# Kernel optimization log

Measured on AMD Instinct MI355X. Metric: run time of the kernel, lower is better.

Reference implementation:

```python
import jax, jax.numpy as jnp
import numpy as np

D = 128          # node feature dim (input_dim)
ATT_NUM = 2      # number of attention heads (att_num)
ATT_TIMES = 2    # attention refinement iterations (att_times)
K = 1            # interact_dim from att_style 'ntn_1'
DIN2 = D * ATT_NUM   # NTN input dim = 256
FMAP = 16        # feature_map_dim
B = 8            # number of graph pairs
N = 100000       # nodes per graph
EPS = 1e-12      # F.normalize eps


def _glorot(key, shape):
    fan_in, fan_out = shape[-1], shape[-2] if len(shape) > 1 else shape[-1]
    std = np.sqrt(2.0 / (fan_in + fan_out)).astype(np.float32)
    return jax.random.normal(key, shape, dtype=jnp.float32) * std


def setup_inputs() -> dict:
    key = jax.random.key(0)
    ks = jax.random.split(key, 16)
    inp = {
        "x1": jax.random.normal(ks[0], (B, N, D), dtype=jnp.float32),
        "x2": jax.random.normal(ks[1], (B, N, D), dtype=jnp.float32),
        # Attention params (stacked over att_num heads)
        "W_att": _glorot(ks[2], (ATT_NUM, D, D)),
        "V_att": _glorot(ks[3], (ATT_NUM, K, 2 * D)),
        "Wt_att": _glorot(ks[4], (ATT_NUM, K, D, D)),
        "U_att": _glorot(ks[5], (ATT_NUM, K, 1)),
        "b_att": jax.random.normal(ks[6], (ATT_NUM, K), dtype=jnp.float32) * 0.1,
        # NTN params
        "V_ntn": _glorot(ks[7], (FMAP, 2 * DIN2)),
        "W_ntn": _glorot(ks[8], (FMAP, DIN2, DIN2)),
        "b_ntn": jax.random.normal(ks[9], (FMAP,), dtype=jnp.float32),
        # projection MLP: 16 -> 8 -> 4 -> 2 -> 1 (Linear, no bias; weight shape (out, in))
        "proj0": _glorot(ks[10], (8, 16)),
        "proj1": _glorot(ks[11], (4, 8)),
        "proj2": _glorot(ks[12], (2, 4)),
        "proj3": _glorot(ks[13], (1, 2)),
    }
    return inp


def _l1_normalize(s, axis):
    return s / jnp.maximum(jnp.sum(jnp.abs(s), axis=axis, keepdims=True), EPS)


def _attention(x, W_att, V_att, Wt_att, U_att, b_att):
    # x: (N, D)  ->  pooled graph embedding (D * ATT_NUM,)
    outs = []
    for i in range(ATT_NUM):
        xc = x
        out = None
        Va, Vb = V_att[i, :, :D], V_att[i, :, D:]   # (K, D) each
        for _ in range(ATT_TIMES):
            h = jnp.tanh(jnp.mean(xc, axis=0) @ W_att[i])        # (D,)
            # NTN-style attention scores, vectorized over all nodes
            s = xc @ Va.T + (Vb @ h)[None, :]                    # (N, K)
            s = s + jnp.einsum('nd,kde,e->nk', xc, Wt_att[i], h)
            s = s + b_att[i][None, :]
            s = _l1_normalize(s, axis=1)
            att = jax.nn.sigmoid(s) @ U_att[i]                   # (N, 1)
            out = att[:, 0] @ xc                                 # (D,)
            xc = xc * att
        outs.append(out)
    return jnp.concatenate(outs)   # (DIN2,)


def _ntn(g1, g2, V_ntn, W_ntn, b_ntn):
    # g1, g2: (DIN2,) -> (FMAP,)
    Va, Vb = V_ntn[:, :DIN2], V_ntn[:, DIN2:]
    s = Va @ g1 + Vb @ g2 + jnp.einsum('fde,d,e->f', W_ntn, g1, g2) + b_ntn
    s = s / jnp.maximum(jnp.sum(jnp.abs(s)), EPS)   # L1 normalize over the single row
    return jax.nn.relu(s)


def reference(x1, x2, W_att, V_att, Wt_att, U_att, b_att,
              V_ntn, W_ntn, b_ntn, proj0, proj1, proj2, proj3):
    def pair_fn(xa, xb):
        g1 = _attention(xa, W_att, V_att, Wt_att, U_att, b_att)
        g2 = _attention(xb, W_att, V_att, Wt_att, U_att, b_att)
        y = _ntn(g1, g2, V_ntn, W_ntn, b_ntn)      # (FMAP,)
        for Wp in (proj0, proj1, proj2, proj3):
            y = Wp @ y
        return y                                    # (1,)
    return jax.vmap(pair_fn)(x1, x2)                # (B, 1) pairwise similarity scores
```

## Files before the change

kernel.cpp:

```cpp
#include <hip/hip_runtime.h>
#include <hip/hip_bf16.h>
#include <math.h>

#define NROWS 100000
#define DIM 128
#define NGRAPH 16
#define NCHUNK 128
#define CHROWS 782
#define EPSV 1e-12f

#define SZ_SUMP (NGRAPH*NCHUNK*DIM)
#define SZ_WV   (NGRAPH*2*DIM)
#define SZ_OP   (NGRAPH*NCHUNK*2*DIM)
#define OFF_SUMP 0
#define OFF_WV1 (OFF_SUMP + SZ_SUMP)
#define OFF_C1  (OFF_WV1 + SZ_WV)
#define OFF_O1P (OFF_C1 + 32)
#define OFF_WV2 (OFF_O1P + SZ_OP)
#define OFF_C2  (OFF_WV2 + SZ_WV)
#define OFF_O2P (OFF_C2 + 32)
#define OFF_S   (OFF_O2P + SZ_OP)

typedef float v4f __attribute__((ext_vector_type(4)));

__device__ __forceinline__ const float* graph_ptr(const float* x1, const float* x2, int g) {
    return (g < 8) ? (x1 + (size_t)g * NROWS * DIM) : (x2 + (size_t)(g - 8) * NROWS * DIM);
}

__device__ __forceinline__ float4 ldnt4(const float* p) {
    v4f v = __builtin_nontemporal_load(reinterpret_cast<const v4f*>(p));
    return make_float4(v.x, v.y, v.z, v.w);
}

__device__ __forceinline__ float4 ld4(const float* p) {
    return *reinterpret_cast<const float4*>(p);
}

__device__ __forceinline__ float red16(float x) {
    int t;
    t = __builtin_amdgcn_update_dpp(0, __float_as_int(x), 0xB1, 0xF, 0xF, true);
    x += __int_as_float(t);
    t = __builtin_amdgcn_update_dpp(0, __float_as_int(x), 0x4E, 0xF, 0xF, true);
    x += __int_as_float(t);
    t = __builtin_amdgcn_update_dpp(0, __float_as_int(x), 0x141, 0xF, 0xF, true);
    x += __int_as_float(t);
    t = __builtin_amdgcn_update_dpp(0, __float_as_int(x), 0x140, 0xF, 0xF, true);
    x += __int_as_float(t);
    return x;
}

__device__ __forceinline__ float dot8(float4 v0, float4 v1, float4 w0, float4 w1) {
    float d = v0.x * w0.x;
    d = fmaf(v0.y, w0.y, d); d = fmaf(v0.z, w0.z, d); d = fmaf(v0.w, w0.w, d);
    d = fmaf(v1.x, w1.x, d); d = fmaf(v1.y, w1.y, d); d = fmaf(v1.z, w1.z, d);
    d = fmaf(v1.w, w1.w, d);
    return d;
}

__device__ __forceinline__ void acc4(float4& a, float f, float4 v) {
    a.x = fmaf(f, v.x, a.x); a.y = fmaf(f, v.y, a.y);
    a.z = fmaf(f, v.z, a.z); a.w = fmaf(f, v.w, a.w);
}

__global__ __launch_bounds__(256, 8) void k_sum(const float* __restrict__ x1,
                                                const float* __restrict__ x2,
                                                float* __restrict__ sump) {
    int g = blockIdx.x >> 7, c = blockIdx.x & (NCHUNK - 1);
    const float* xg = graph_ptr(x1, x2, g);
    int lane = threadIdx.x & 31, grp = threadIdx.x >> 5;
    int col = lane * 4;
    float ax = 0.f, ay = 0.f, az = 0.f, aw = 0.f;
    int r0 = c * CHROWS, r1 = min(r0 + CHROWS, NROWS);
    int r = r0 + grp;
    for (; r + 24 < r1; r += 32) {
        float4 a = ldnt4(xg + (size_t)r * DIM + col);
        float4 b = ldnt4(xg + (size_t)(r + 8) * DIM + col);
        float4 d = ldnt4(xg + (size_t)(r + 16) * DIM + col);
        float4 e = ldnt4(xg + (size_t)(r + 24) * DIM + col);
        ax += a.x; ay += a.y; az += a.z; aw += a.w;
        ax += b.x; ay += b.y; az += b.z; aw += b.w;
        ax += d.x; ay += d.y; az += d.z; aw += d.w;
        ax += e.x; ay += e.y; az += e.z; aw += e.w;
    }
    for (; r < r1; r += 8) {
        float4 a = ldnt4(xg + (size_t)r * DIM + col);
        ax += a.x; ay += a.y; az += a.z; aw += a.w;
    }
    __shared__ float4 lds[256];
    lds[threadIdx.x] = make_float4(ax, ay, az, aw);
    __syncthreads();
    if (threadIdx.x < 32) {
        float4 t = lds[threadIdx.x];
        for (int k = 1; k < 8; ++k) {
            float4 o = lds[k * 32 + threadIdx.x];
            t.x += o.x; t.y += o.y; t.z += o.z; t.w += o.w;
        }
        *reinterpret_cast<float4*>(sump + ((size_t)g * NCHUNK + c) * DIM + threadIdx.x * 4) = t;
    }
}

__global__ __launch_bounds__(256) void k_prep(const float* __restrict__ src, int phase,
                                              const float* __restrict__ W_att,
                                              const float* __restrict__ V_att,
                                              const float* __restrict__ Wt_att,
                                              const float* __restrict__ b_att,
                                              float* __restrict__ wv, float* __restrict__ cc) {
    int g = blockIdx.x >> 1, i = blockIdx.x & 1;
    int tid = threadIdx.x, t = tid & 127, half = tid >> 7;
    __shared__ float mean[DIM], h[DIM], red2[256];
    __shared__ float wt[DIM][DIM + 1];
    const float* Wt = Wt_att + (size_t)i * DIM * DIM;
    for (int idx = tid; idx < DIM * DIM; idx += 256)
        wt[idx >> 7][idx & 127] = Wt[idx];
    float s = 0.f;
    if (phase == 1) {
        for (int c = half; c < NCHUNK; c += 2) s += src[((size_t)g * NCHUNK + c) * DIM + t];
    } else {
        for (int c = half; c < NCHUNK; c += 2) s += src[(((size_t)g * NCHUNK + c) * 2 + i) * DIM + t];
    }
    red2[tid] = s; __syncthreads();
    if (half == 0) mean[t] = (red2[t] + red2[t + 128]) * (1.f / (float)NROWS);
    __syncthreads();
    const float* W = W_att + (size_t)i * DIM * DIM;
    float hv = 0.f;
    for (int d = half * 64; d < half * 64 + 64; ++d) hv = fmaf(mean[d], W[d * DIM + t], hv);
    red2[tid] = hv; __syncthreads();
    if (half == 0) h[t] = tanhf(red2[t] + red2[t + 128]);
    __syncthreads();
    float w = 0.f;
    for (int e = half * 64; e < half * 64 + 64; ++e) w = fmaf(wt[t][e], h[e], w);
    red2[tid] = w; __syncthreads();
    const float* Va = V_att + (size_t)i * 2 * DIM;
    if (half == 0) wv[((size_t)g * 2 + i) * DIM + t] = Va[t] + red2[t] + red2[t + 128];
    __syncthreads();
    if (half == 0) red2[t] = Va[DIM + t] * h[t];
    __syncthreads();
    for (int k = 64; k; k >>= 1) {
        if (tid < k) red2[tid] += red2[tid + k];
        __syncthreads();
    }
    if (tid == 0) cc[g * 2 + i] = red2[0] + b_att[i];
}

__device__ __forceinline__ void body2(float4 v0, float4 v1,
                                      float4 w0a, float4 w0b, float4 w1a, float4 w1b,
                                      float cc0, float cc1,
                                      float ap0, float an0, float ap1, float an1,
                                      float4& a0l, float4& a0h, float4& a1l, float4& a1h) {
    float d0 = red16(dot8(v0, v1, w0a, w0b));
    float d1 = red16(dot8(v0, v1, w1a, w1b));
    float at0 = (d0 + cc0 >= 0.f) ? ap0 : an0;
    float at1 = (d1 + cc1 >= 0.f) ? ap1 : an1;
    acc4(a0l, at0, v0); acc4(a0h, at0, v1);
    acc4(a1l, at1, v0); acc4(a1h, at1, v1);
}

__global__ __launch_bounds__(256, 6) void k_pass2(const float* __restrict__ x1,
                                                  const float* __restrict__ x2,
                                                  const float* __restrict__ wv1,
                                                  const float* __restrict__ c1,
                                                  const float* __restrict__ U_att,
                                                  float* __restrict__ o1p) {
    int g = blockIdx.x >> 7, c = blockIdx.x & (NCHUNK - 1);
    const float* xg = graph_ptr(x1, x2, g);
    int tid = threadIdx.x;
    int l16 = tid & 15, slot = tid >> 4;
    int cb = l16 * 4;
    float4 w0a = ld4(wv1 + ((size_t)g * 2 + 0) * DIM + cb);
    float4 w0b = ld4(wv1 + ((size_t)g * 2 + 0) * DIM + 64 + cb);
    float4 w1a = ld4(wv1 + ((size_t)g * 2 + 1) * DIM + cb);
    float4 w1b = ld4(wv1 + ((size_t)g * 2 + 1) * DIM + 64 + cb);
    float cc0 = c1[g * 2 + 0], cc1 = c1[g * 2 + 1];
    float u0 = U_att[0], u1 = U_att[1];
    float sp = 1.f / (1.f + expf(-1.f)), sn = 1.f / (1.f + expf(1.f));
    float ap0 = u0 * sp, an0 = u0 * sn, ap1 = u1 * sp, an1 = u1 * sn;
    float4 a0l = make_float4(0, 0, 0, 0), a0h = make_float4(0, 0, 0, 0);
    float4 a1l = make_float4(0, 0, 0, 0), a1h = make_float4(0, 0, 0, 0);
    int r0 = c * CHROWS, r1 = min(r0 + CHROWS, NROWS);
    int r = r0 + slot;
    for (; r + 16 < r1; r += 32) {
        const float* p = xg + (size_t)r * DIM + cb;
        const float* q = xg + (size_t)(r + 16) * DIM + cb;
        float4 v0 = ldnt4(p), v1 = ldnt4(p + 64);
        float4 y0 = ldnt4(q), y1 = ldnt4(q + 64);
        body2(v0, v1, w0a, w0b, w1a, w1b, cc0, cc1, ap0, an0, ap1, an1, a0l, a0h, a1l, a1h);
        body2(y0, y1, w0a, w0b, w1a, w1b, cc0, cc1, ap0, an0, ap1, an1, a0l, a0h, a1l, a1h);
    }
    for (; r < r1; r += 16) {
        const float* p = xg + (size_t)r * DIM + cb;
        float4 v0 = ldnt4(p), v1 = ldnt4(p + 64);
        body2(v0, v1, w0a, w0b, w1a, w1b, cc0, cc1, ap0, an0, ap1, an1, a0l, a0h, a1l, a1h);
    }
    __shared__ float red[2][16][DIM];
    *reinterpret_cast<float4*>(&red[0][slot][cb]) = a0l;
    *reinterpret_cast<float4*>(&red[0][slot][64 + cb]) = a0h;
    *reinterpret_cast<float4*>(&red[1][slot][cb]) = a1l;
    *reinterpret_cast<float4*>(&red[1][slot][64 + cb]) = a1h;
    __syncthreads();
    int i = tid >> 7, d = tid & 127;
    float s = 0.f;
    #pragma unroll
    for (int k = 0; k < 16; ++k) s += red[i][k][d];
    o1p[(((size_t)g * NCHUNK + c) * 2 + i) * DIM + d] = s;
}

__device__ __forceinline__ void body3(float4 v0, float4 v1,
                                      float4 wA0a, float4 wA0b, float4 wA1a, float4 wA1b,
                                      float4 wB0a, float4 wB0b, float4 wB1a, float4 wB1b,
                                      float cA0, float cA1, float cB0, float cB1,
                                      float ap0, float an0, float ap1, float an1,
                                      float4& a0l, float4& a0h, float4& a1l, float4& a1h) {
    float dA0 = red16(dot8(v0, v1, wA0a, wA0b));
    float dA1 = red16(dot8(v0, v1, wA1a, wA1b));
    float dB0 = red16(dot8(v0, v1, wB0a, wB0b));
    float dB1 = red16(dot8(v0, v1, wB1a, wB1b));
    float at10 = (dA0 + cA0 >= 0.f) ? ap0 : an0;
    float at11 = (dA1 + cA1 >= 0.f) ? ap1 : an1;
    float at20 = (fmaf(at10, dB0, cB0) >= 0.f) ? ap0 : an0;
    float at21 = (fmaf(at11, dB1, cB1) >= 0.f) ? ap1 : an1;
    float f0 = at10 * at20, f1 = at11 * at21;
    acc4(a0l, f0, v0); acc4(a0h, f0, v1);
    acc4(a1l, f1, v0); acc4(a1h, f1, v1);
}

__global__ __launch_bounds__(256, 6) void k_pass3(const float* __restrict__ x1,
                                                  const float* __restrict__ x2,
                                                  const float* __restrict__ wv1,
                                                  const float* __restrict__ c1,
                                                  const float* __restrict__ wv2,
                                                  const float* __restrict__ c2,
                                                  const float* __restrict__ U_att,
                                                  float* __restrict__ o2p) {
    int g = blockIdx.x >> 7, c = blockIdx.x & (NCHUNK - 1);
    const float* xg = graph_ptr(x1, x2, g);
    int tid = threadIdx.x;
    int l16 = tid & 15, slot = tid >> 4;
    int cb = l16 * 4;
    float4 wA0a = ld4(wv1 + ((size_t)g * 2 + 0) * DIM + cb);
    float4 wA0b = ld4(wv1 + ((size_t)g * 2 + 0) * DIM + 64 + cb);
    float4 wA1a = ld4(wv1 + ((size_t)g * 2 + 1) * DIM + cb);
    float4 wA1b = ld4(wv1 + ((size_t)g * 2 + 1) * DIM + 64 + cb);
    float4 wB0a = ld4(wv2 + ((size_t)g * 2 + 0) * DIM + cb);
    float4 wB0b = ld4(wv2 + ((size_t)g * 2 + 0) * DIM + 64 + cb);
    float4 wB1a = ld4(wv2 + ((size_t)g * 2 + 1) * DIM + cb);
    float4 wB1b = ld4(wv2 + ((size_t)g * 2 + 1) * DIM + 64 + cb);
    float cA0 = c1[g * 2 + 0], cA1 = c1[g * 2 + 1];
    float cB0 = c2[g * 2 + 0], cB1 = c2[g * 2 + 1];
    float u0 = U_att[0], u1 = U_att[1];
    float sp = 1.f / (1.f + expf(-1.f)), sn = 1.f / (1.f + expf(1.f));
    float ap0 = u0 * sp, an0 = u0 * sn, ap1 = u1 * sp, an1 = u1 * sn;
    float4 a0l = make_float4(0, 0, 0, 0), a0h = make_float4(0, 0, 0, 0);
    float4 a1l = make_float4(0, 0, 0, 0), a1h = make_float4(0, 0, 0, 0);
    int r0 = c * CHROWS, r1 = min(r0 + CHROWS, NROWS);
    int r = r0 + slot;
    for (; r + 16 < r1; r += 32) {
        const float* p = xg + (size_t)r * DIM + cb;
        const float* q = xg + (size_t)(r + 16) * DIM + cb;
        float4 v0 = ldnt4(p), v1 = ldnt4(p + 64);
        float4 y0 = ldnt4(q), y1 = ldnt4(q + 64);
        body3(v0, v1, wA0a, wA0b, wA1a, wA1b, wB0a, wB0b, wB1a, wB1b,
              cA0, cA1, cB0, cB1, ap0, an0, ap1, an1, a0l, a0h, a1l, a1h);
        body3(y0, y1, wA0a, wA0b, wA1a, wA1b, wB0a, wB0b, wB1a, wB1b,
              cA0, cA1, cB0, cB1, ap0, an0, ap1, an1, a0l, a0h, a1l, a1h);
    }
    for (; r < r1; r += 16) {
        const float* p = xg + (size_t)r * DIM + cb;
        float4 v0 = ldnt4(p), v1 = ldnt4(p + 64);
        body3(v0, v1, wA0a, wA0b, wA1a, wA1b, wB0a, wB0b, wB1a, wB1b,
              cA0, cA1, cB0, cB1, ap0, an0, ap1, an1, a0l, a0h, a1l, a1h);
    }
    __shared__ float red[2][16][DIM];
    *reinterpret_cast<float4*>(&red[0][slot][cb]) = a0l;
    *reinterpret_cast<float4*>(&red[0][slot][64 + cb]) = a0h;
    *reinterpret_cast<float4*>(&red[1][slot][cb]) = a1l;
    *reinterpret_cast<float4*>(&red[1][slot][64 + cb]) = a1h;
    __syncthreads();
    int i = tid >> 7, d = tid & 127;
    float s = 0.f;
    #pragma unroll
    for (int k = 0; k < 16; ++k) s += red[i][k][d];
    o2p[(((size_t)g * NCHUNK + c) * 2 + i) * DIM + d] = s;
}

__global__ __launch_bounds__(256) void k_ntn(const float* __restrict__ o2p,
                                             const float* __restrict__ V_ntn,
                                             const float* __restrict__ W_ntn,
                                             const float* __restrict__ b_ntn,
                                             float* __restrict__ sout) {
    int b = blockIdx.x >> 4, f = blockIdx.x & 15;
    int e = threadIdx.x;
    __shared__ float g1s[256], g2s[256], red[256];
    int i = e >> 7, d = e & 127;
    float s1 = 0.f, s2 = 0.f;
    for (int c = 0; c < NCHUNK; ++c) {
        s1 += o2p[(((size_t)b * NCHUNK + c) * 2 + i) * DIM + d];
        s2 += o2p[(((size_t)(8 + b) * NCHUNK + c) * 2 + i) * DIM + d];
    }
    g1s[e] = s1; g2s[e] = s2;
    __syncthreads();
    const float* Wf = W_ntn + (size_t)f * 256 * 256;
    float acc = 0.f;
    for (int dd = 0; dd < 256; ++dd) acc = fmaf(Wf[(size_t)dd * 256 + e], g1s[dd], acc);
    float p = acc * g2s[e];
    p = fmaf(V_ntn[(size_t)f * 512 + e], g1s[e], p);
    p = fmaf(V_ntn[(size_t)f * 512 + 256 + e], g2s[e], p);
    red[e] = p;
    __syncthreads();
    for (int k = 128; k; k >>= 1) {
        if (e < k) red[e] += red[e + k];
        __syncthreads();
    }
    if (e == 0) sout[b * 16 + f] = red[0] + b_ntn[f];
}

__global__ __launch_bounds__(64) void k_out(const float* __restrict__ sout,
                                            const float* __restrict__ p0,
                                            const float* __restrict__ p1,
                                            const float* __restrict__ p2,
                                            const float* __restrict__ p3,
                                            float* __restrict__ out) {
    int b = blockIdx.x;
    if (threadIdx.x != 0) return;
    float s[16]; float l1 = 0.f;
    for (int f = 0; f < 16; ++f) { s[f] = sout[b * 16 + f]; l1 += fabsf(s[f]); }
    float inv = 1.f / fmaxf(l1, EPSV);
    float y[16];
    for (int f = 0; f < 16; ++f) { float t = s[f] * inv; y[f] = t > 0.f ? t : 0.f; }
    float v2[4], v1[8], P[16];
    for (int j = 0; j < 4; ++j) v2[j] = p3[0] * p2[j] + p3[1] * p2[4 + j];
    for (int j = 0; j < 8; ++j) { float a = 0.f; for (int k = 0; k < 4; ++k) a = fmaf(v2[k], p1[k * 8 + j], a); v1[j] = a; }
    for (int j = 0; j < 16; ++j) { float a = 0.f; for (int k = 0; k < 8; ++k) a = fmaf(v1[k], p0[k * 16 + j], a); P[j] = a; }
    float o = 0.f;
    for (int f = 0; f < 16; ++f) o = fmaf(P[f], y[f], o);
    out[b] = o;
}

extern "C" void kernel_launch(void* const* d_in, const int* in_sizes, int n_in,
                              void* d_out, int out_size, void* d_ws, size_t ws_size,
                              hipStream_t stream) {
    const float* x1    = (const float*)d_in[0];
    const float* x2    = (const float*)d_in[1];
    const float* W_att = (const float*)d_in[2];
    const float* V_att = (const float*)d_in[3];
    const float* Wt_att= (const float*)d_in[4];
    const float* U_att = (const float*)d_in[5];
    const float* b_att = (const float*)d_in[6];
    const float* V_ntn = (const float*)d_in[7];
    const float* W_ntn = (const float*)d_in[8];
    const float* b_ntn = (const float*)d_in[9];
    const float* p0    = (const float*)d_in[10];
    const float* p1    = (const float*)d_in[11];
    const float* p2    = (const float*)d_in[12];
    const float* p3    = (const float*)d_in[13];
    float* ws  = (float*)d_ws;
    float* out = (float*)d_out;

    k_sum<<<NGRAPH * NCHUNK, 256, 0, stream>>>(x1, x2, ws + OFF_SUMP);
    k_prep<<<NGRAPH * 2, 256, 0, stream>>>(ws + OFF_SUMP, 1, W_att, V_att, Wt_att, b_att,
                                           ws + OFF_WV1, ws + OFF_C1);
    k_pass2<<<NGRAPH * NCHUNK, 256, 0, stream>>>(x1, x2, ws + OFF_WV1, ws + OFF_C1, U_att,
                                                 ws + OFF_O1P);
    k_prep<<<NGRAPH * 2, 256, 0, stream>>>(ws + OFF_O1P, 2, W_att, V_att, Wt_att, b_att,
                                           ws + OFF_WV2, ws + OFF_C2);
    k_pass3<<<NGRAPH * NCHUNK, 256, 0, stream>>>(x1, x2, ws + OFF_WV1, ws + OFF_C1,
                                                 ws + OFF_WV2, ws + OFF_C2, U_att,
                                                 ws + OFF_O2P);
    k_ntn<<<8 * 16, 256, 0, stream>>>(ws + OFF_O2P, V_ntn, W_ntn, b_ntn, ws + OFF_S);
    k_out<<<8, 64, 0, stream>>>(ws + OFF_S, p0, p1, p2, p3, out);
}
```

Baseline: 486.4 us.

## Fuse pipeline into one cooperative kernel with grid syncs and fixed-point atomics

Replaces the seven-kernel sequence with one cooperative persistent kernel of 1024 blocks. Grid-wide syncs separate the sum, prep, pass2, prep, pass3, NTN and output stages. Per-chunk partial sums are reduced through 64-bit fixed-point atomics, which stay deterministic, instead of workspace arrays. Non-temporal loads are swapped for plain loads, possibly so some of the 3x re-read of x can hit in cache. The aim is to remove launch gaps and separate reduction passes. The risks are grid-sync cost, reduced occupancy at launch_bounds(256,4), fixed-point quantization error, and a fallback path if the cooperative launch fails.

```diff
diff --git a/kernel.cpp b/kernel.cpp
--- a/kernel.cpp
+++ b/kernel.cpp
@@ -1,14 +1,17 @@
 #include <hip/hip_runtime.h>
+#include <hip/hip_cooperative_groups.h>
 #include <hip/hip_bf16.h>
 #include <math.h>
+
+namespace cg = cooperative_groups;
 
 #define NROWS 100000
 #define DIM 128
 #define NGRAPH 16
+#define EPSV 1e-12f
+
 #define NCHUNK 128
 #define CHROWS 782
-#define EPSV 1e-12f
-
 #define SZ_SUMP (NGRAPH*NCHUNK*DIM)
 #define SZ_WV   (NGRAPH*2*DIM)
 #define SZ_OP   (NGRAPH*NCHUNK*2*DIM)
@@ -21,15 +24,15 @@
 #define OFF_O2P (OFF_C2 + 32)
 #define OFF_S   (OFF_O2P + SZ_OP)
 
-typedef float v4f __attribute__((ext_vector_type(4)));
+#define MCH 64
+#define MCHR 1563
+#define MEGA_F0 2000000
+#define SCALE26 67108864.0
+#define INV26 (1.0/67108864.0)
+#define INV26N (1.0/(67108864.0*100000.0))
 
 __device__ __forceinline__ const float* graph_ptr(const float* x1, const float* x2, int g) {
     return (g < 8) ? (x1 + (size_t)g * NROWS * DIM) : (x2 + (size_t)(g - 8) * NROWS * DIM);
-}
-
-__device__ __forceinline__ float4 ldnt4(const float* p) {
-    v4f v = __builtin_nontemporal_load(reinterpret_cast<const v4f*>(p));
-    return make_float4(v.x, v.y, v.z, v.w);
 }
 
 __device__ __forceinline__ float4 ld4(const float* p) {
@@ -62,86 +65,6 @@
     a.z = fmaf(f, v.z, a.z); a.w = fmaf(f, v.w, a.w);
 }
 
-__global__ __launch_bounds__(256, 8) void k_sum(const float* __restrict__ x1,
-                                                const float* __restrict__ x2,
-                                                float* __restrict__ sump) {
-    int g = blockIdx.x >> 7, c = blockIdx.x & (NCHUNK - 1);
-    const float* xg = graph_ptr(x1, x2, g);
-    int lane = threadIdx.x & 31, grp = threadIdx.x >> 5;
-    int col = lane * 4;
-    float ax = 0.f, ay = 0.f, az = 0.f, aw = 0.f;
-    int r0 = c * CHROWS, r1 = min(r0 + CHROWS, NROWS);
-    int r = r0 + grp;
-    for (; r + 24 < r1; r += 32) {
-        float4 a = ldnt4(xg + (size_t)r * DIM + col);
-        float4 b = ldnt4(xg + (size_t)(r + 8) * DIM + col);
-        float4 d = ldnt4(xg + (size_t)(r + 16) * DIM + col);
-        float4 e = ldnt4(xg + (size_t)(r + 24) * DIM + col);
-        ax += a.x; ay += a.y; az += a.z; aw += a.w;
-        ax += b.x; ay += b.y; az += b.z; aw += b.w;
-        ax += d.x; ay += d.y; az += d.z; aw += d.w;
-        ax += e.x; ay += e.y; az += e.z; aw += e.w;
-    }
-    for (; r < r1; r += 8) {
-        float4 a = ldnt4(xg + (size_t)r * DIM + col);
-        ax += a.x; ay += a.y; az += a.z; aw += a.w;
-    }
-    __shared__ float4 lds[256];
-    lds[threadIdx.x] = make_float4(ax, ay, az, aw);
-    __syncthreads();
-    if (threadIdx.x < 32) {
-        float4 t = lds[threadIdx.x];
-        for (int k = 1; k < 8; ++k) {
-            float4 o = lds[k * 32 + threadIdx.x];
-            t.x += o.x; t.y += o.y; t.z += o.z; t.w += o.w;
-        }
-        *reinterpret_cast<float4*>(sump + ((size_t)g * NCHUNK + c) * DIM + threadIdx.x * 4) = t;
-    }
-}
-
-__global__ __launch_bounds__(256) void k_prep(const float* __restrict__ src, int phase,
-                                              const float* __restrict__ W_att,
-                                              const float* __restrict__ V_att,
-                                              const float* __restrict__ Wt_att,
-                                              const float* __restrict__ b_att,
-                                              float* __restrict__ wv, float* __restrict__ cc) {
-    int g = blockIdx.x >> 1, i = blockIdx.x & 1;
-    int tid = threadIdx.x, t = tid & 127, half = tid >> 7;
-    __shared__ float mean[DIM], h[DIM], red2[256];
-    __shared__ float wt[DIM][DIM + 1];
-    const float* Wt = Wt_att + (size_t)i * DIM * DIM;
-    for (int idx = tid; idx < DIM * DIM; idx += 256)
-        wt[idx >> 7][idx & 127] = Wt[idx];
-    float s = 0.f;
-    if (phase == 1) {
-        for (int c = half; c < NCHUNK; c += 2) s += src[((size_t)g * NCHUNK + c) * DIM + t];
-    } else {
-        for (int c = half; c < NCHUNK; c += 2) s += src[(((size_t)g * NCHUNK + c) * 2 + i) * DIM + t];
-    }
-    red2[tid] = s; __syncthreads();
-    if (half == 0) mean[t] = (red2[t] + red2[t + 128]) * (1.f / (float)NROWS);
-    __syncthreads();
-    const float* W = W_att + (size_t)i * DIM * DIM;
-    float hv = 0.f;
-    for (int d = half * 64; d < half * 64 + 64; ++d) hv = fmaf(mean[d], W[d * DIM + t], hv);
-    red2[tid] = hv; __syncthreads();
-    if (half == 0) h[t] = tanhf(red2[t] + red2[t + 128]);
-    __syncthreads();
-    float w = 0.f;
-    for (int e = half * 64; e < half * 64 + 64; ++e) w = fmaf(wt[t][e], h[e], w);
-    red2[tid] = w; __syncthreads();
-    const float* Va = V_att + (size_t)i * 2 * DIM;
-    if (half == 0) wv[((size_t)g * 2 + i) * DIM + t] = Va[t] + red2[t] + red2[t + 128];
-    __syncthreads();
-    if (half == 0) red2[t] = Va[DIM + t] * h[t];
-    __syncthreads();
-    for (int k = 64; k; k >>= 1) {
-        if (tid < k) red2[tid] += red2[tid + k];
-        __syncthreads();
-    }
-    if (tid == 0) cc[g * 2 + i] = red2[0] + b_att[i];
-}
-
 __device__ __forceinline__ void body2(float4 v0, float4 v1,
                                       float4 w0a, float4 w0b, float4 w1a, float4 w1b,
                                       float cc0, float cc1,
@@ -153,55 +76,6 @@
     float at1 = (d1 + cc1 >= 0.f) ? ap1 : an1;
     acc4(a0l, at0, v0); acc4(a0h, at0, v1);
     acc4(a1l, at1, v0); acc4(a1h, at1, v1);
-}
-
-__global__ __launch_bounds__(256, 6) void k_pass2(const float* __restrict__ x1,
-                                                  const float* __restrict__ x2,
-                                                  const float* __restrict__ wv1,
-                                                  const float* __restrict__ c1,
-                                                  const float* __restrict__ U_att,
-                                                  float* __restrict__ o1p) {
-    int g = blockIdx.x >> 7, c = blockIdx.x & (NCHUNK - 1);
-    const float* xg = graph_ptr(x1, x2, g);
-    int tid = threadIdx.x;
-    int l16 = tid & 15, slot = tid >> 4;
-    int cb = l16 * 4;
-    float4 w0a = ld4(wv1 + ((size_t)g * 2 + 0) * DIM + cb);
-    float4 w0b = ld4(wv1 + ((size_t)g * 2 + 0) * DIM + 64 + cb);
-    float4 w1a = ld4(wv1 + ((size_t)g * 2 + 1) * DIM + cb);
-    float4 w1b = ld4(wv1 + ((size_t)g * 2 + 1) * DIM + 64 + cb);
-    float cc0 = c1[g * 2 + 0], cc1 = c1[g * 2 + 1];
-    float u0 = U_att[0], u1 = U_att[1];
-    float sp = 1.f / (1.f + expf(-1.f)), sn = 1.f / (1.f + expf(1.f));
-    float ap0 = u0 * sp, an0 = u0 * sn, ap1 = u1 * sp, an1 = u1 * sn;
-    float4 a0l = make_float4(0, 0, 0, 0), a0h = make_float4(0, 0, 0, 0);
-    float4 a1l = make_float4(0, 0, 0, 0), a1h = make_float4(0, 0, 0, 0);
-    int r0 = c * CHROWS, r1 = min(r0 + CHROWS, NROWS);
-    int r = r0 + slot;
-    for (; r + 16 < r1; r += 32) {
-        const float* p = xg + (size_t)r * DIM + cb;
-        const float* q = xg + (size_t)(r + 16) * DIM + cb;
-        float4 v0 = ldnt4(p), v1 = ldnt4(p + 64);
-        float4 y0 = ldnt4(q), y1 = ldnt4(q + 64);
-        body2(v0, v1, w0a, w0b, w1a, w1b, cc0, cc1, ap0, an0, ap1, an1, a0l, a0h, a1l, a1h);
-        body2(y0, y1, w0a, w0b, w1a, w1b, cc0, cc1, ap0, an0, ap1, an1, a0l, a0h, a1l, a1h);
-    }
-    for (; r < r1; r += 16) {
-        const float* p = xg + (size_t)r * DIM + cb;
-        float4 v0 = ldnt4(p), v1 = ldnt4(p + 64);
-        body2(v0, v1, w0a, w0b, w1a, w1b, cc0, cc1, ap0, an0, ap1, an1, a0l, a0h, a1l, a1h);
-    }
-    __shared__ float red[2][16][DIM];
-    *reinterpret_cast<float4*>(&red[0][slot][cb]) = a0l;
-    *reinterpret_cast<float4*>(&red[0][slot][64 + cb]) = a0h;
-    *reinterpret_cast<float4*>(&red[1][slot][cb]) = a1l;
-    *reinterpret_cast<float4*>(&red[1][slot][64 + cb]) = a1h;
-    __syncthreads();
-    int i = tid >> 7, d = tid & 127;
-    float s = 0.f;
-    #pragma unroll
-    for (int k = 0; k < 16; ++k) s += red[i][k][d];
-    o1p[(((size_t)g * NCHUNK + c) * 2 + i) * DIM + d] = s;
 }
 
 __device__ __forceinline__ void body3(float4 v0, float4 v1,
@@ -223,19 +97,373 @@
     acc4(a1l, f1, v0); acc4(a1h, f1, v1);
 }
 
-__global__ __launch_bounds__(256, 6) void k_pass3(const float* __restrict__ x1,
-                                                  const float* __restrict__ x2,
-                                                  const float* __restrict__ wv1,
-                                                  const float* __restrict__ c1,
-                                                  const float* __restrict__ wv2,
-                                                  const float* __restrict__ c2,
-                                                  const float* __restrict__ U_att,
-                                                  float* __restrict__ o2p) {
+__device__ __forceinline__ void atomic_acc26(long long* p, float v) {
+    long long q = (long long)rint((double)v * SCALE26);
+    atomicAdd((unsigned long long*)p, (unsigned long long)q);
+}
+
+
+struct KParams {
+    const float *x1, *x2, *W, *V, *Wt, *U, *bA, *Vn, *Wn, *bn, *p0, *p1, *p2, *p3;
+    float *out, *ws;
+};
+
+__device__ void prep_dev(const KParams& P, float* smem, int g, int i, int tid,
+                         const long long* src, float* wv, float* cc) {
+    float* mean = smem;
+    float* h    = smem + 128;
+    float* red2 = smem + 256;
+    int t = tid & 127;
+    if (tid < 128) mean[t] = (float)((double)src[t] * INV26N);
+    __syncthreads();
+    float hv = 0.f;
+    if (tid < 128) {
+        const float* W = P.W + (size_t)i * DIM * DIM;
+        for (int d = 0; d < DIM; ++d) hv = fmaf(mean[d], W[d * DIM + t], hv);
+        h[t] = tanhf(hv);
+    }
+    __syncthreads();
+    if (tid < 128) {
+        const float* Wt = P.Wt + (size_t)i * DIM * DIM;
+        const float* Va = P.V + (size_t)i * 2 * DIM;
+        float w = Va[t];
+        for (int e = 0; e < DIM; ++e) w = fmaf(Wt[t * DIM + e], h[e], w);
+        wv[((size_t)g * 2 + i) * DIM + t] = w;
+        red2[t] = Va[DIM + t] * h[t];
+    }
+    __syncthreads();
+    for (int k = 64; k; k >>= 1) {
+        if (tid < k) red2[tid] += red2[tid + k];
+        __syncthreads();
+    }
+    if (tid == 0) cc[g * 2 + i] = red2[0] + P.bA[i];
+}
+
+__global__ __launch_bounds__(256, 4) void k_mega(KParams P) {
+    cg::grid_group grid = cg::this_grid();
+    __shared__ __align__(16) float smem[4096];
+    const int bid = blockIdx.x, tid = threadIdx.x;
+
+    float* wv1  = P.ws + MEGA_F0;
+    float* c1   = wv1 + 4096;
+    float* wv2  = c1 + 32;
+    float* c2   = wv2 + 4096;
+    float* sout = c2 + 32;
+    long long* acc     = (long long*)(P.ws + MEGA_F0 + 8448);
+    long long* sum_acc = acc;
+    long long* o1_acc  = acc + 2048;
+    long long* g_acc   = acc + 2048 + 4096;
+
+    { int idx = bid * 256 + tid; if (idx < 10240) acc[idx] = 0; }
+    grid.sync();
+
+    const int g = bid >> 6, c = bid & (MCH - 1);
+    const float* xg = graph_ptr(P.x1, P.x2, g);
+    const int r0 = c * MCHR, r1 = min(r0 + MCHR, NROWS);
+
+    {
+        int lane = tid & 31, grp = tid >> 5, col = lane * 4;
+        float ax = 0.f, ay = 0.f, az = 0.f, aw = 0.f;
+        int r = r0 + grp;
+        for (; r + 8 < r1; r += 16) {
+            float4 a = ld4(xg + (size_t)r * DIM + col);
+            float4 b = ld4(xg + (size_t)(r + 8) * DIM + col);
+            ax += a.x; ay += a.y; az += a.z; aw += a.w;
+            ax += b.x; ay += b.y; az += b.z; aw += b.w;
+        }
+        if (r < r1) {
+            float4 a = ld4(xg + (size_t)r * DIM + col);
+            ax += a.x; ay += a.y; az += a.z; aw += a.w;
+        }
+        float4* l4 = (float4*)smem;
+        l4[tid] = make_float4(ax, ay, az, aw);
+        __syncthreads();
+        if (tid < 32) {
+            float4 t = l4[tid];
+            for (int k = 1; k < 8; ++k) {
+                float4 o = l4[k * 32 + tid];
+                t.x += o.x; t.y += o.y; t.z += o.z; t.w += o.w;
+            }
+            int d = tid * 4;
+            atomic_acc26(&sum_acc[g * DIM + d + 0], t.x);
+            atomic_acc26(&sum_acc[g * DIM + d + 1], t.y);
+            atomic_acc26(&sum_acc[g * DIM + d + 2], t.z);
+            atomic_acc26(&sum_acc[g * DIM + d + 3], t.w);
+        }
+    }
+    grid.sync();
+
+    if (bid < 32) prep_dev(P, smem, bid >> 1, bid & 1, tid, &sum_acc[(bid >> 1) * DIM], wv1, c1);
+    grid.sync();
+
+    {
+        int l16 = tid & 15, slot = tid >> 4, cb = l16 * 4;
+        float4 w0a = ld4(wv1 + ((size_t)g * 2 + 0) * DIM + cb);
+        float4 w0b = ld4(wv1 + ((size_t)g * 2 + 0) * DIM + 64 + cb);
+        float4 w1a = ld4(wv1 + ((size_t)g * 2 + 1) * DIM + cb);
+        float4 w1b = ld4(wv1 + ((size_t)g * 2 + 1) * DIM + 64 + cb);
+        float cc0 = c1[g * 2 + 0], cc1 = c1[g * 2 + 1];
+        float u0 = P.U[0], u1 = P.U[1];
+        float sp = 1.f / (1.f + expf(-1.f)), sn = 1.f / (1.f + expf(1.f));
+        float ap0 = u0 * sp, an0 = u0 * sn, ap1 = u1 * sp, an1 = u1 * sn;
+        float4 a0l = make_float4(0, 0, 0, 0), a0h = make_float4(0, 0, 0, 0);
+        float4 a1l = make_float4(0, 0, 0, 0), a1h = make_float4(0, 0, 0, 0);
+        int r = r0 + slot;
+        for (; r + 16 < r1; r += 32) {
+            const float* p = xg + (size_t)r * DIM + cb;
+            const float* q = xg + (size_t)(r + 16) * DIM + cb;
+            float4 v0 = ld4(p), v1 = ld4(p + 64);
+            float4 y0 = ld4(q), y1 = ld4(q + 64);
+            body2(v0, v1, w0a, w0b, w1a, w1b, cc0, cc1, ap0, an0, ap1, an1, a0l, a0h, a1l, a1h);
+            body2(y0, y1, w0a, w0b, w1a, w1b, cc0, cc1, ap0, an0, ap1, an1, a0l, a0h, a1l, a1h);
+        }
+        for (; r < r1; r += 16) {
+            const float* p = xg + (size_t)r * DIM + cb;
+            float4 v0 = ld4(p), v1 = ld4(p + 64);
+            body2(v0, v1, w0a, w0b, w1a, w1b, cc0, cc1, ap0, an0, ap1, an1, a0l, a0h, a1l, a1h);
+        }
+        __syncthreads();
+        float* red = smem;
+        *(float4*)&red[(0 * 16 + slot) * DIM + cb] = a0l;
+        *(float4*)&red[(0 * 16 + slot) * DIM + 64 + cb] = a0h;
+        *(float4*)&red[(1 * 16 + slot) * DIM + cb] = a1l;
+        *(float4*)&red[(1 * 16 + slot) * DIM + 64 + cb] = a1h;
+        __syncthreads();
+        int i = tid >> 7, d = tid & 127;
+        float s = 0.f;
+        #pragma unroll
+        for (int k = 0; k < 16; ++k) s += red[(i * 16 + k) * DIM + d];
+        atomic_acc26(&o1_acc[((size_t)g * 2 + i) * DIM + d], s);
+    }
+    grid.sync();
+
+    if (bid < 32) prep_dev(P, smem, bid >> 1, bid & 1, tid,
+                           &o1_acc[((size_t)(bid >> 1) * 2 + (bid & 1)) * DIM], wv2, c2);
+    grid.sync();
+
+    {
+        int l16 = tid & 15, slot = tid >> 4, cb = l16 * 4;
+        float4 wA0a = ld4(wv1 + ((size_t)g * 2 + 0) * DIM + cb);
+        float4 wA0b = ld4(wv1 + ((size_t)g * 2 + 0) * DIM + 64 + cb);
+        float4 wA1a = ld4(wv1 + ((size_t)g * 2 + 1) * DIM + cb);
+        float4 wA1b = ld4(wv1 + ((size_t)g * 2 + 1) * DIM + 64 + cb);
+        float4 wB0a = ld4(wv2 + ((size_t)g * 2 + 0) * DIM + cb);
+        float4 wB0b = ld4(wv2 + ((size_t)g * 2 + 0) * DIM + 64 + cb);
+        float4 wB1a = ld4(wv2 + ((size_t)g * 2 + 1) * DIM + cb);
+        float4 wB1b = ld4(wv2 + ((size_t)g * 2 + 1) * DIM + 64 + cb);
+        float cA0 = c1[g * 2 + 0], cA1 = c1[g * 2 + 1];
+        float cB0 = c2[g * 2 + 0], cB1 = c2[g * 2 + 1];
+        float u0 = P.U[0], u1 = P.U[1];
+        float sp = 1.f / (1.f + expf(-1.f)), sn = 1.f / (1.f + expf(1.f));
+        float ap0 = u0 * sp, an0 = u0 * sn, ap1 = u1 * sp, an1 = u1 * sn;
+        float4 a0l = make_float4(0, 0, 0, 0), a0h = make_float4(0, 0, 0, 0);
+        float4 a1l = make_float4(0, 0, 0, 0), a1h = make_float4(0, 0, 0, 0);
+        int r = r0 + slot;
+        for (; r + 16 < r1; r += 32) {
+            const float* p = xg + (size_t)r * DIM + cb;
+            const float* q = xg + (size_t)(r + 16) * DIM + cb;
+            float4 v0 = ld4(p), v1 = ld4(p + 64);
+            float4 y0 = ld4(q), y1 = ld4(q + 64);
+            body3(v0, v1, wA0a, wA0b, wA1a, wA1b, wB0a, wB0b, wB1a, wB1b,
+                  cA0, cA1, cB0, cB1, ap0, an0, ap1, an1, a0l, a0h, a1l, a1h);
+            body3(y0, y1, wA0a, wA0b, wA1a, wA1b, wB0a, wB0b, wB1a, wB1b,
+                  cA0, cA1, cB0, cB1, ap0, an0, ap1, an1, a0l, a0h, a1l, a1h);
+        }
+        for (; r < r1; r += 16) {
+            const float* p = xg + (size_t)r * DIM + cb;
+            float4 v0 = ld4(p), v1 = ld4(p + 64);
+            body3(v0, v1, wA0a, wA0b, wA1a, wA1b, wB0a, wB0b, wB1a, wB1b,
+                  cA0, cA1, cB0, cB1, ap0, an0, ap1, an1, a0l, a0h, a1l, a1h);
+        }
+        __syncthreads();
+        float* red = smem;
+        *(float4*)&red[(0 * 16 + slot) * DIM + cb] = a0l;
+        *(float4*)&red[(0 * 16 + slot) * DIM + 64 + cb] = a0h;
+        *(float4*)&red[(1 * 16 + slot) * DIM + cb] = a1l;
+        *(float4*)&red[(1 * 16 + slot) * DIM + 64 + cb] = a1h;
+        __syncthreads();
+        int i = tid >> 7, d = tid & 127;
+        float s = 0.f;
+        #pragma unroll
+        for (int k = 0; k < 16; ++k) s += red[(i * 16 + k) * DIM + d];
+        atomic_acc26(&g_acc[((size_t)g * 2 + i) * DIM + d], s);
+    }
+    grid.sync();
+
+    if (bid < 128) {
+        int b = bid >> 4, f = bid & 15, e = tid;
+        float* g1s = smem; float* g2s = smem + 256; float* red = smem + 512;
+        int i = e >> 7, d = e & 127;
+        g1s[e] = (float)((double)g_acc[((size_t)b * 2 + i) * DIM + d] * INV26);
+        g2s[e] = (float)((double)g_acc[((size_t)(8 + b) * 2 + i) * DIM + d] * INV26);
+        __syncthreads();
+        const float* Wf = P.Wn + (size_t)f * 256 * 256;
+        float a = 0.f;
+        for (int dd = 0; dd < 256; ++dd) a = fmaf(Wf[(size_t)dd * 256 + e], g1s[dd], a);
+        float p = a * g2s[e];
+        p = fmaf(P.Vn[(size_t)f * 512 + e], g1s[e], p);
+        p = fmaf(P.Vn[(size_t)f * 512 + 256 + e], g2s[e], p);
+        red[e] = p;
+        __syncthreads();
+        for (int k = 128; k; k >>= 1) {
+            if (e < k) red[e] += red[e + k];
+            __syncthreads();
+        }
+        if (e == 0) sout[b * 16 + f] = red[0] + P.bn[f];
+    }
+    grid.sync();
+
+    if (bid < 8 && tid == 0) {
+        int b = bid;
+        float s[16]; float l1 = 0.f;
+        for (int f = 0; f < 16; ++f) { s[f] = sout[b * 16 + f]; l1 += fabsf(s[f]); }
+        float inv = 1.f / fmaxf(l1, EPSV);
+        float y[16];
+        for (int f = 0; f < 16; ++f) { float t = s[f] * inv; y[f] = t > 0.f ? t : 0.f; }
+        float v2[4], v1[8], Pr[16];
+        for (int j = 0; j < 4; ++j) v2[j] = P.p3[0] * P.p2[j] + P.p3[1] * P.p2[4 + j];
+        for (int j = 0; j < 8; ++j) { float a = 0.f; for (int k = 0; k < 4; ++k) a = fmaf(v2[k], P.p1[k * 8 + j], a); v1[j] = a; }
+        for (int j = 0; j < 16; ++j) { float a = 0.f; for (int k = 0; k < 8; ++k) a = fmaf(v1[k], P.p0[k * 16 + j], a); Pr[j] = a; }
+        float o = 0.f;
+        for (int f = 0; f < 16; ++f) o = fmaf(Pr[f], y[f], o);
+        P.out[b] = o;
+    }
+}
+
+
+__global__ __launch_bounds__(256) void k_sum(const float* __restrict__ x1,
+                                             const float* __restrict__ x2,
+                                             float* __restrict__ sump) {
+    int g = blockIdx.x >> 7, c = blockIdx.x & (NCHUNK - 1);
+    const float* xg = graph_ptr(x1, x2, g);
+    int lane = threadIdx.x & 31, grp = threadIdx.x >> 5;
+    int col = lane * 4;
+    float ax = 0.f, ay = 0.f, az = 0.f, aw = 0.f;
+    int r0 = c * CHROWS, r1 = min(r0 + CHROWS, NROWS);
+    int r = r0 + grp;
+    for (; r + 8 < r1; r += 16) {
+        float4 a = ld4(xg + (size_t)r * DIM + col);
+        float4 b = ld4(xg + (size_t)(r + 8) * DIM + col);
+        ax += a.x; ay += a.y; az += a.z; aw += a.w;
+        ax += b.x; ay += b.y; az += b.z; aw += b.w;
+    }
+    if (r < r1) {
+        float4 a = ld4(xg + (size_t)r * DIM + col);
+        ax += a.x; ay += a.y; az += a.z; aw += a.w;
+    }
+    __shared__ float4 lds[256];
+    lds[threadIdx.x] = make_float4(ax, ay, az, aw);
+    __syncthreads();
+    if (threadIdx.x < 32) {
+        float4 t = lds[threadIdx.x];
+        for (int k = 1; k < 8; ++k) {
+            float4 o = lds[k * 32 + threadIdx.x];
+            t.x += o.x; t.y += o.y; t.z += o.z; t.w += o.w;
+        }
+        *reinterpret_cast<float4*>(sump + ((size_t)g * NCHUNK + c) * DIM + threadIdx.x * 4) = t;
+    }
+}
+
+__global__ __launch_bounds__(256) void k_prep(const float* __restrict__ src, int phase,
+                                              const float* __restrict__ W_att,
+                                              const float* __restrict__ V_att,
+                                              const float* __restrict__ Wt_att,
+                                              const float* __restrict__ b_att,
+                                              float* __restrict__ wv, float* __restrict__ cc) {
+    int g = blockIdx.x >> 1, i = blockIdx.x & 1;
+    int tid = threadIdx.x, t = tid & 127, half = tid >> 7;
+    __shared__ float mean[DIM], h[DIM], red2[256];
+    float s = 0.f;
+    if (phase == 1) {
+        for (int c = half; c < NCHUNK; c += 2) s += src[((size_t)g * NCHUNK + c) * DIM + t];
+    } else {
+        for (int c = half; c < NCHUNK; c += 2) s += src[(((size_t)g * NCHUNK + c) * 2 + i) * DIM + t];
+    }
+    red2[tid] = s; __syncthreads();
+    if (half == 0) mean[t] = (red2[t] + red2[t + 128]) * (1.f / (float)NROWS);
+    __syncthreads();
+    const float* W = W_att + (size_t)i * DIM * DIM;
+    float hv = 0.f;
+    for (int d = half * 64; d < half * 64 + 64; ++d) hv = fmaf(mean[d], W[d * DIM + t], hv);
+    red2[tid] = hv; __syncthreads();
+    if (half == 0) h[t] = tanhf(red2[t] + red2[t + 128]);
+    __syncthreads();
+    const float* Wt = Wt_att + (size_t)i * DIM * DIM;
+    float w = 0.f;
+    for (int e = half * 64; e < half * 64 + 64; ++e) w = fmaf(Wt[t * DIM + e], h[e], w);
+    red2[tid] = w; __syncthreads();
+    const float* Va = V_att + (size_t)i * 2 * DIM;
+    if (half == 0) wv[((size_t)g * 2 + i) * DIM + t] = Va[t] + red2[t] + red2[t + 128];
+    __syncthreads();
+    if (half == 0) red2[t] = Va[DIM + t] * h[t];
+    __syncthreads();
+    for (int k = 64; k; k >>= 1) {
+        if (tid < k) red2[tid] += red2[tid + k];
+        __syncthreads();
+    }
+    if (tid == 0) cc[g * 2 + i] = red2[0] + b_att[i];
+}
+
+__global__ __launch_bounds__(256) void k_pass2(const float* __restrict__ x1,
+                                               const float* __restrict__ x2,
+                                               const float* __restrict__ wv1,
+                                               const float* __restrict__ c1,
+                                               const float* __restrict__ U_att,
+                                               float* __restrict__ o1p) {
     int g = blockIdx.x >> 7, c = blockIdx.x & (NCHUNK - 1);
     const float* xg = graph_ptr(x1, x2, g);
     int tid = threadIdx.x;
-    int l16 = tid & 15, slot = tid >> 4;
-    int cb = l16 * 4;
+    int l16 = tid & 15, slot = tid >> 4, cb = l16 * 4;
+    float4 w0a = ld4(wv1 + ((size_t)g * 2 + 0) * DIM + cb);
+    float4 w0b = ld4(wv1 + ((size_t)g * 2 + 0) * DIM + 64 + cb);
+    float4 w1a = ld4(wv1 + ((size_t)g * 2 + 1) * DIM + cb);
+    float4 w1b = ld4(wv1 + ((size_t)g * 2 + 1) * DIM + 64 + cb);
+    float cc0 = c1[g * 2 + 0], cc1 = c1[g * 2 + 1];
+    float u0 = U_att[0], u1 = U_att[1];
+    float sp = 1.f / (1.f + expf(-1.f)), sn = 1.f / (1.f + expf(1.f));
+    float ap0 = u0 * sp, an0 = u0 * sn, ap1 = u1 * sp, an1 = u1 * sn;
+    float4 a0l = make_float4(0, 0, 0, 0), a0h = make_float4(0, 0, 0, 0);
+    float4 a1l = make_float4(0, 0, 0, 0), a1h = make_float4(0, 0, 0, 0);
+    int r0 = c * CHROWS, r1 = min(r0 + CHROWS, NROWS);
+    int r = r0 + slot;
+    for (; r + 16 < r1; r += 32) {
+        const float* p = xg + (size_t)r * DIM + cb;
+        const float* q = xg + (size_t)(r + 16) * DIM + cb;
+        float4 v0 = ld4(p), v1 = ld4(p + 64);
+        float4 y0 = ld4(q), y1 = ld4(q + 64);
+        body2(v0, v1, w0a, w0b, w1a, w1b, cc0, cc1, ap0, an0, ap1, an1, a0l, a0h, a1l, a1h);
+        body2(y0, y1, w0a, w0b, w1a, w1b, cc0, cc1, ap0, an0, ap1, an1, a0l, a0h, a1l, a1h);
+    }
+    for (; r < r1; r += 16) {
+        const float* p = xg + (size_t)r * DIM + cb;
+        float4 v0 = ld4(p), v1 = ld4(p + 64);
+        body2(v0, v1, w0a, w0b, w1a, w1b, cc0, cc1, ap0, an0, ap1, an1, a0l, a0h, a1l, a1h);
+    }
+    __shared__ float red[2][16][DIM];
+    *reinterpret_cast<float4*>(&red[0][slot][cb]) = a0l;
+    *reinterpret_cast<float4*>(&red[0][slot][64 + cb]) = a0h;
+    *reinterpret_cast<float4*>(&red[1][slot][cb]) = a1l;
+    *reinterpret_cast<float4*>(&red[1][slot][64 + cb]) = a1h;
+    __syncthreads();
+    int i = tid >> 7, d = tid & 127;
+    float s = 0.f;
+    #pragma unroll
+    for (int k = 0; k < 16; ++k) s += red[i][k][d];
+    o1p[(((size_t)g * NCHUNK + c) * 2 + i) * DIM + d] = s;
+}
+
+__global__ __launch_bounds__(256) void k_pass3(const float* __restrict__ x1,
+                                               const float* __restrict__ x2,
+                                               const float* __restrict__ wv1,
+                                               const float* __restrict__ c1,
+                                               const float* __restrict__ wv2,
+                                               const float* __restrict__ c2,
+                                               const float* __restrict__ U_att,
+                                               float* __restrict__ o2p) {
+    int g = blockIdx.x >> 7, c = blockIdx.x & (NCHUNK - 1);
+    const float* xg = graph_ptr(x1, x2, g);
+    int tid = threadIdx.x;
+    int l16 = tid & 15, slot = tid >> 4, cb = l16 * 4;
     float4 wA0a = ld4(wv1 + ((size_t)g * 2 + 0) * DIM + cb);
     float4 wA0b = ld4(wv1 + ((size_t)g * 2 + 0) * DIM + 64 + cb);
     float4 wA1a = ld4(wv1 + ((size_t)g * 2 + 1) * DIM + cb);
@@ -256,8 +484,8 @@
     for (; r + 16 < r1; r += 32) {
         const float* p = xg + (size_t)r * DIM + cb;
         const float* q = xg + (size_t)(r + 16) * DIM + cb;
-        float4 v0 = ldnt4(p), v1 = ldnt4(p + 64);
-        float4 y0 = ldnt4(q), y1 = ldnt4(q + 64);
+        float4 v0 = ld4(p), v1 = ld4(p + 64);
+        float4 y0 = ld4(q), y1 = ld4(q + 64);
         body3(v0, v1, wA0a, wA0b, wA1a, wA1b, wB0a, wB0b, wB1a, wB1b,
               cA0, cA1, cB0, cB1, ap0, an0, ap1, an1, a0l, a0h, a1l, a1h);
         body3(y0, y1, wA0a, wA0b, wA1a, wA1b, wB0a, wB0b, wB1a, wB1b,
@@ -265,7 +493,7 @@
     }
     for (; r < r1; r += 16) {
         const float* p = xg + (size_t)r * DIM + cb;
-        float4 v0 = ldnt4(p), v1 = ldnt4(p + 64);
+        float4 v0 = ld4(p), v1 = ld4(p + 64);
         body3(v0, v1, wA0a, wA0b, wA1a, wA1b, wB0a, wB0b, wB1a, wB1b,
               cA0, cA1, cB0, cB1, ap0, an0, ap1, an1, a0l, a0h, a1l, a1h);
     }
@@ -355,16 +583,24 @@
     float* ws  = (float*)d_ws;
     float* out = (float*)d_out;
 
-    k_sum<<<NGRAPH * NCHUNK, 256, 0, stream>>>(x1, x2, ws + OFF_SUMP);
-    k_prep<<<NGRAPH * 2, 256, 0, stream>>>(ws + OFF_SUMP, 1, W_att, V_att, Wt_att, b_att,
-                                           ws + OFF_WV1, ws + OFF_C1);
-    k_pass2<<<NGRAPH * NCHUNK, 256, 0, stream>>>(x1, x2, ws + OFF_WV1, ws + OFF_C1, U_att,
-                                                 ws + OFF_O1P);
-    k_prep<<<NGRAPH * 2, 256, 0, stream>>>(ws + OFF_O1P, 2, W_att, V_att, Wt_att, b_att,
-                                           ws + OFF_WV2, ws + OFF_C2);
-    k_pass3<<<NGRAPH * NCHUNK, 256, 0, stream>>>(x1, x2, ws + OFF_WV1, ws + OFF_C1,
-                                                 ws + OFF_WV2, ws + OFF_C2, U_att,
-                                                 ws + OFF_O2P);
-    k_ntn<<<8 * 16, 256, 0, stream>>>(ws + OFF_O2P, V_ntn, W_ntn, b_ntn, ws + OFF_S);
-    k_out<<<8, 64, 0, stream>>>(ws + OFF_S, p0, p1, p2, p3, out);
-}
+    KParams P{x1, x2, W_att, V_att, Wt_att, U_att, b_att,
+              V_ntn, W_ntn, b_ntn, p0, p1, p2, p3, out, ws};
+    void* args[] = {&P};
+    hipError_t err = hipLaunchCooperativeKernel((const void*)k_mega, dim3(16 * MCH),
+                                                dim3(256), args, 0, stream);
+    if (err != hipSuccess) {
+        (void)hipGetLastError();
+        k_sum<<<NGRAPH * NCHUNK, 256, 0, stream>>>(x1, x2, ws + OFF_SUMP);
+        k_prep<<<NGRAPH * 2, 256, 0, stream>>>(ws + OFF_SUMP, 1, W_att, V_att, Wt_att, b_att,
+                                               ws + OFF_WV1, ws + OFF_C1);
+        k_pass2<<<NGRAPH * NCHUNK, 256, 0, stream>>>(x1, x2, ws + OFF_WV1, ws + OFF_C1, U_att,
+                                                     ws + OFF_O1P);
+        k_prep<<<NGRAPH * 2, 256, 0, stream>>>(ws + OFF_O1P, 2, W_att, V_att, Wt_att, b_att,
+                                               ws + OFF_WV2, ws + OFF_C2);
+        k_pass3<<<NGRAPH * NCHUNK, 256, 0, stream>>>(x1, x2, ws + OFF_WV1, ws + OFF_C1,
+                                                     ws + OFF_WV2, ws + OFF_C2, U_att,
+                                                     ws + OFF_O2P);
+        k_ntn<<<8 * 16, 256, 0, stream>>>(ws + OFF_O2P, V_ntn, W_ntn, b_ntn, ws + OFF_S);
+        k_out<<<8, 64, 0, stream>>>(ws + OFF_S, p0, p1, p2, p3, out);
+    }
+}
```

Result: slower. 1.252 ms (+157.3%).
